# Performance work log

Measured on AMD Instinct MI355X. Metric: run time of the kernel, lower is better.

Reference implementation:

```python
import jax, jax.numpy as jnp
import numpy as np

B, HIST, T_TOTAL = 16, 8, 16
C, IN_DIM, EMB, HID = 1000, 16, 32, 64
E = 16000
D_BASE = 2
ED = D_BASE + 3                # edge_dim = 5
IN_CONV = IN_DIM - 1 + EMB + 2  # 49
IN_GRU = IN_CONV + HID          # 113
N = B * C
U10_MEAN, U10_STD = 0.5, 3.0
V10_MEAN, V10_STD = -0.3, 3.0
TWO_PI = 2.0 * np.pi


def _wind_dir(u, v):
    # metpy wind_direction in radians: 90deg - atan2(-v,-u), wrapped to (0, 2pi], calm -> 0
    d = jnp.pi / 2 - jnp.arctan2(-v, -u)
    d = jnp.where(d <= 0, d + TWO_PI, d)
    return jnp.where(jnp.hypot(u, v) == 0, 0.0, d)


def setup_inputs():
    key = jax.random.key(0)
    ks = jax.random.split(key, 32)
    X = jax.random.normal(ks[0], (B, T_TOTAL, C, IN_DIM), jnp.float32)
    node_ids = jnp.broadcast_to(jnp.arange(C, dtype=jnp.float32), (B, T_TOTAL, C))
    X = X.at[..., -1].set(node_ids)  # last column = node id (embedding index)
    y = jax.random.normal(ks[1], (B, T_TOTAL, C, 1), jnp.float32)
    edge_indices = jax.random.randint(ks[2], (2, E), 0, C, jnp.int32)
    dist = jax.random.uniform(ks[3], (E,), jnp.float32, 10.0, 100.0)
    direc = jax.random.uniform(ks[4], (E,), jnp.float32, 0.0, TWO_PI)
    edge_attr0 = jnp.stack([dist, direc], axis=-1)

    def lin(k, fin, fout):
        s = 1.0 / np.sqrt(fin)
        return jax.random.uniform(k, (fin, fout), jnp.float32, -s, s)

    def bias(k, fout):
        return jax.random.normal(k, (fout,), jnp.float32) * 0.01

    return {
        'X': X, 'y': y, 'edge_attr0': edge_attr0,
        'emb_table': jax.random.normal(ks[5], (C, EMB), jnp.float32),
        'Wq': lin(ks[6], IN_CONV, HID), 'bq': bias(ks[7], HID),
        'Wk': lin(ks[8], IN_CONV, HID), 'bk': bias(ks[9], HID),
        'Wv': lin(ks[10], IN_CONV, HID), 'bv': bias(ks[11], HID),
        'We': lin(ks[12], ED, HID), 'be': bias(ks[13], HID),
        'Wskip': lin(ks[14], IN_CONV, HID), 'bskip': bias(ks[15], HID),
        'W_ih': lin(ks[16], IN_GRU, 3 * HID).T, 'b_ih': bias(ks[17], 3 * HID),
        'W_hh': lin(ks[18], HID, 3 * HID).T, 'b_hh': bias(ks[19], 3 * HID),
        'Wout': lin(ks[20], HID, 1), 'bout': bias(ks[21], 1),
        'edge_indices': edge_indices,
    }


def reference(X, y, edge_attr0, emb_table, Wq, bq, Wk, bk, Wv, bv, We, be,
              Wskip, bskip, W_ih, b_ih, W_hh, b_hh, Wout, bout, edge_indices):
    offs = jnp.arange(B, dtype=jnp.int32) * C
    # batched-graph indices, flattened batch-major (b*E+e) exactly as the source
    SRC = (edge_indices[0][None, :] + offs[:, None]).reshape(-1)
    DST = (edge_indices[1][None, :] + offs[:, None]).reshape(-1)
    src_nodes = edge_indices[0]
    base = edge_attr0[src_nodes]  # [E, 2] (dist, dir); faithful to edge_attr[src] quirk
    inv_sqrt_d = 1.0 / np.sqrt(HID)

    def step(carry, xs):
        hn, xn = carry
        Xt, yt = xs  # [B,C,IN_DIM], [B,C,1]
        ids = Xt[..., -1].astype(jnp.int32)
        emb = emb_table[ids]                               # [B,C,EMB]
        feats = Xt[..., :-1]
        x = jnp.concatenate([xn, yt, feats, emb], axis=-1)  # [B,C,IN_CONV]
        # vectorized wind physics (replaces the per-edge CPU loop)
        u10 = feats[..., -2] * U10_STD + U10_MEAN
        v10 = feats[..., -1] * V10_STD + V10_MEAN
        speed = jnp.hypot(u10, v10)
        wind = jnp.stack([speed, _wind_dir(u10, v10)], axis=-1)      # [B,C,2]
        w_e = jnp.transpose(wind[:, src_nodes, :], (1, 0, 2))        # [E,B,2]
        base_e = jnp.broadcast_to(base[:, None, :], (E, B, D_BASE))
        attr4 = jnp.concatenate([base_e, w_e], axis=-1)              # [E,B,4]
        theta = jnp.abs(attr4[..., 1] - attr4[..., 3])
        adv = jax.nn.relu(3.0 * attr4[..., 2] * jnp.cos(theta) / attr4[..., 0])
        # edge-major flatten (e*B+b), paired with batch-major SRC/DST as in source
        edge_attr = jnp.concatenate([attr4, adv[..., None]], axis=-1).reshape(E * B, ED)
        # TransformerConv, heads=1, eval (no dropout)
        xf = x.reshape(N, IN_CONV)
        q = xf @ Wq + bq
        kk = xf @ Wk + bk
        vv = xf @ Wv + bv
        e_emb = edge_attr @ We + be
        k_e = kk[SRC] + e_emb
        v_e = vv[SRC] + e_emb
        alpha = jnp.sum(q[DST] * k_e, axis=-1) * inv_sqrt_d
        m = jax.ops.segment_max(alpha, DST, num_segments=N)
        a = jnp.exp(alpha - m[DST])
        s = jax.ops.segment_sum(a, DST, num_segments=N)
        p = a / s[DST]
        out = jax.ops.segment_sum(p[:, None] * v_e, DST, num_segments=N)
        out = out + xf @ Wskip + bskip
        x_gcn = jax.nn.sigmoid(out).reshape(B, C, HID)
        x2 = jnp.concatenate([x, x_gcn], axis=-1).reshape(N, IN_GRU)
        # GRUCell
        gi = x2 @ W_ih.T + b_ih
        gh = hn @ W_hh.T + b_hh
        i_r, i_z, i_n = jnp.split(gi, 3, axis=-1)
        h_r, h_z, h_n = jnp.split(gh, 3, axis=-1)
        r = jax.nn.sigmoid(i_r + h_r)
        z = jax.nn.sigmoid(i_z + h_z)
        n = jnp.tanh(i_n + r * h_n)
        hn_new = (1.0 - z) * n + z * hn
        xn_new = hn_new.reshape(B, C, HID) @ Wout + bout
        return (hn_new, xn_new), None

    hn0 = jnp.zeros((N, HID), jnp.float32)
    xn0 = jnp.zeros((B, C, 1), jnp.float32)
    xs = (jnp.swapaxes(X[:, :HIST], 0, 1), jnp.swapaxes(y[:, :HIST], 0, 1))
    (hn, xn), _ = jax.lax.scan(step, (hn0, xn0), xs)
    return hn, xn
```

## Files before the change

### kernel.cpp

```cpp
#include <hip/hip_runtime.h>
#include <math.h>

#define B_ 16
#define T_TOT 16
#define C_ 1000
#define N_ 16000
#define E_ 16000
#define HID 64
#define EMB 32
#define IN_DIM 16
#define XF 17
#define HIST 8
#define SXP 160
#define HOFF 96
#define SHP 168
#define SGP 268
#define Q_ 16

typedef __attribute__((ext_vector_type(8))) short bf16x8;
typedef __attribute__((ext_vector_type(4))) float f32x4;

__device__ __forceinline__ float sigmoidf_(float x) { return 1.f / (1.f + expf(-x)); }

__global__ void k_init(float* __restrict__ hn, float* __restrict__ xn, int* __restrict__ cnt) {
  int total = N_ * HID + N_ + C_;
  for (int i = blockIdx.x * 256 + threadIdx.x; i < total; i += gridDim.x * 256) {
    if (i < N_ * HID) hn[i] = 0.f;
    else if (i < N_ * HID + N_) xn[i - N_ * HID] = 0.f;
    else cnt[i - N_ * HID - N_] = 0;
  }
}

__global__ void k_prep(const float* __restrict__ W_ih, const float* __restrict__ W_hh,
                       unsigned short* __restrict__ WBhi, unsigned short* __restrict__ WBlo,
                       float* __restrict__ WihT2) {
  int i = blockIdx.x * 256 + threadIdx.x;
  if (i < 30720) {
    const int j = i & 7;
    const int l = (i >> 3) & 63;
    const int ksnt = i >> 9;
    const int ks = ksnt % 5, nt = ksnt / 5;
    const int k = ks * 32 + (l >> 4) * 8 + j;
    const int g = nt * 16 + (l & 15);
    float w = 0.f;
    if (k < 17) w = W_ih[g * 113 + k];
    else if (k < 81) w = W_ih[g * 113 + 49 + (k - 17)];
    else if (k >= HOFF) w = W_hh[g * 64 + (k - HOFF)];
    const unsigned ub = __float_as_uint(w);
    const float hif = __uint_as_float(ub & 0xffff0000u);
    WBhi[i] = (unsigned short)(ub >> 16);
    WBlo[i] = (unsigned short)(__float_as_uint(w - hif) >> 16);
  } else if (i < 30720 + 32 * 192) {
    int i2 = i - 30720;
    int j2 = i2 / 192, g = i2 - j2 * 192;
    WihT2[i2] = W_ih[g * 113 + 17 + j2];
  }
}

__global__ __launch_bounds__(256) void k_embfold(
    const float* __restrict__ emb_table,
    const float* __restrict__ Wq, const float* __restrict__ Wk,
    const float* __restrict__ Wv, const float* __restrict__ Wskip,
    const float* __restrict__ WihT2,
    float* __restrict__ embW, float* __restrict__ gihemb) {
  __shared__ float se[EMB];
  const int c = blockIdx.x;
  const int t = threadIdx.x;
  if (t < EMB) se[t] = emb_table[c * EMB + t];
  __syncthreads();
  const int mat = t >> 6, h = t & 63;
  const float* Wm = (mat == 0) ? Wq : (mat == 1) ? Wk : (mat == 2) ? Wv : Wskip;
  float acc = 0.f;
#pragma unroll
  for (int j = 0; j < EMB; ++j) acc = fmaf(se[j], Wm[(17 + j) * HID + h], acc);
  embW[c * 256 + t] = acc;
  if (t < 192) {
    float a2 = 0.f;
#pragma unroll
    for (int j = 0; j < EMB; ++j) a2 = fmaf(se[j], WihT2[j * 192 + t], a2);
    gihemb[c * 192 + t] = a2;
  }
}

__global__ __launch_bounds__(256) void k_count(const int* __restrict__ dst,
                                               int* __restrict__ qcnt, int* __restrict__ cnt) {
  const int gw = (blockIdx.x * 256 + threadIdx.x) >> 6;
  const int lane = threadIdx.x & 63;
  const int d = gw >> 4, q = gw & (Q_ - 1);
  const int e0 = q * (E_ / Q_);
  int cur = 0;
  for (int base = 0; base < E_ / Q_; base += 64) {
    const bool in = (base + lane) < (E_ / Q_);
    const int e = e0 + (in ? base + lane : 0);
    cur += __popcll(__ballot(in && (dst[e] == d)));
  }
  if (lane == 0) { qcnt[(d << 4) + q] = cur; atomicAdd(&cnt[d], cur); }
}

__global__ __launch_bounds__(1024) void k_scan(const int* __restrict__ cnt, int* __restrict__ rowptr) {
  __shared__ int s[1024];
  int t = threadIdx.x;
  s[t] = (t < C_) ? cnt[t] : 0;
  __syncthreads();
  for (int off = 1; off < 1024; off <<= 1) {
    int v = (t >= off) ? s[t - off] : 0;
    __syncthreads();
    s[t] += v;
    __syncthreads();
  }
  if (t < C_) rowptr[t + 1] = s[t];
  if (t == 0) rowptr[0] = 0;
}

__global__ __launch_bounds__(256) void k_scatter(const int* __restrict__ dst,
                                                 const int* __restrict__ rowptr,
                                                 const int* __restrict__ qcnt,
                                                 int* __restrict__ csr_e) {
  const int gw = (blockIdx.x * 256 + threadIdx.x) >> 6;
  const int lane = threadIdx.x & 63;
  const int d = gw >> 4, q = gw & (Q_ - 1);
  int cur = rowptr[d];
  for (int qq = 0; qq < q; ++qq) cur += qcnt[(d << 4) + qq];
  const int e0 = q * (E_ / Q_);
  for (int base = 0; base < E_ / Q_; base += 64) {
    const bool in = (base + lane) < (E_ / Q_);
    const int e = e0 + (in ? base + lane : 0);
    const bool pred = in && (dst[e] == d);
    const unsigned long long mask = __ballot(pred);
    if (pred) csr_e[cur + __popcll(mask & ((1ull << lane) - 1))] = e;
    cur += __popcll(mask);
  }
}

__global__ __launch_bounds__(256) void k_pack(const int* __restrict__ src,
                                              const int* __restrict__ csr_e,
                                              const float* __restrict__ ea0,
                                              int4* __restrict__ pack) {
  const int idx = blockIdx.x * 256 + threadIdx.x;
  const int b = idx / E_, j = idx - b * E_;
  const int e = csr_e[j];
  const int se = src[b * 1000 + (e >> 4)];
  int4 rec;
  rec.x = b * C_ + src[e];
  rec.y = (e & 15) * C_ + se;
  rec.z = __float_as_int(ea0[2 * se]);
  rec.w = __float_as_int(ea0[2 * se + 1]);
  pack[idx] = rec;
}

__global__ __launch_bounds__(256) void k_node_pre(
    const float* __restrict__ X, const float* __restrict__ y,
    const float* __restrict__ embW,
    const float* __restrict__ Wk, const float* __restrict__ bk,
    const float* __restrict__ Wv, const float* __restrict__ bv,
    const float* __restrict__ xn_prev,
    float* __restrict__ k, float* __restrict__ v, float2* __restrict__ wind, int t)
{
  __shared__ float sx[4][XF];
  const int local = threadIdx.x >> 6;
  const int h = threadIdx.x & 63;
  const int n = blockIdx.x * 4 + local;
  const int b = n / C_, c = n % C_;
  const float* Xrow = X + (((b * T_TOT + t) * C_ + c) * IN_DIM);

  if (h == 0)       sx[local][0] = xn_prev[n];
  else if (h == 1)  sx[local][1] = y[(b * T_TOT + t) * C_ + c];
  else if (h <= 16) sx[local][h] = Xrow[h - 2];
  if (h == 0) {
    float u10 = Xrow[13] * 3.0f + 0.5f;
    float v10 = Xrow[14] * 3.0f - 0.3f;
    float sp = hypotf(u10, v10);
    float dd = 1.5707963267948966f - atan2f(-v10, -u10);
    if (dd <= 0.f) dd += 6.283185307179586f;
    if (sp == 0.f) dd = 0.f;
    wind[n] = make_float2(sp, dd);
  }
  __syncthreads();

  const float* eW = embW + c * 256;
  float ak = bk[h] + eW[64 + h];
  float av = bv[h] + eW[128 + h];
#pragma unroll
  for (int j = 0; j < XF; ++j) {
    const float xv = sx[local][j];
    ak = fmaf(xv, Wk[j * HID + h], ak);
    av = fmaf(xv, Wv[j * HID + h], av);
  }
  k[(size_t)n * HID + h] = ak;
  v[(size_t)n * HID + h] = av;
}

__global__ __launch_bounds__(256, 4) void k_node_main(
    const int* __restrict__ rowptr, const int4* __restrict__ pack,
    const float* __restrict__ X, const float* __restrict__ y,
    const float* __restrict__ xn_prev,
    const float* __restrict__ embW, const float* __restrict__ gihemb,
    const float* __restrict__ Wq, const float* __restrict__ bq,
    const float* __restrict__ Wskip, const float* __restrict__ bskip,
    const float* __restrict__ Wk, const float* __restrict__ bk,
    const float* __restrict__ Wv, const float* __restrict__ bv,
    const float* __restrict__ We, const float* __restrict__ be,
    const float* __restrict__ kR, const float* __restrict__ vR, const float2* __restrict__ windR,
    float* __restrict__ kW, float* __restrict__ vW, float2* __restrict__ windW,
    const unsigned short* __restrict__ WBhi, const unsigned short* __restrict__ WBlo,
    const float* __restrict__ b_ih, const float* __restrict__ b_hh,
    const float* __restrict__ Wout, const float* __restrict__ bout,
    const float* __restrict__ hn_in, float* __restrict__ hn_out, float* __restrict__ xn_out,
    int t, int last)
{
  __shared__ float sxh[16 * SXP];
  __shared__ unsigned short sxhH[16 * SHP];
  __shared__ unsigned short sxhL[16 * SHP];
  __shared__ float sg[16 * SGP];

  const int h = threadIdx.x & 63;
  const int wv = threadIdx.x >> 6;
  const int grp = h >> 4, t16 = h & 15;
  const int gbase = h & 48;
  const int lb = ((int)blockIdx.x & 7) * 125 + ((int)blockIdx.x >> 3);
  const int nb0 = wv * 4;
  const int nloc = nb0 + grp;
  const int n = lb * 16 + nloc;
  const int b = n / C_, d = n % C_;

  const int r0 = rowptr[d];
  const int deg = rowptr[d + 1] - r0;
  const int4* packb = pack + (size_t)b * E_;

#pragma unroll 1
  for (int i = 0; i < 4; ++i) {
    const int nl = nb0 + i;
    const int ng = lb * 16 + nl;
    const int bb = ng / C_, cc = ng % C_;
    const float* Xrow = X + (((size_t)(bb * T_TOT + t) * C_ + cc) * IN_DIM);
    float* row = &sxh[nl * SXP];
    if (h == 0)       row[0] = xn_prev[ng];
    else if (h == 1)  row[1] = y[(size_t)(bb * T_TOT + t) * C_ + cc];
    else if (h <= 16) row[h] = Xrow[h - 2];
  }

  float4 qv4, sk4, pA, pB;
  {
    const float* eW = embW + d * 256;
    {
      const float4 bq4 = *(const float4*)(bq + t16 * 4);
      const float4 eq4 = *(const float4*)(eW + t16 * 4);
      qv4 = make_float4(bq4.x + eq4.x, bq4.y + eq4.y, bq4.z + eq4.z, bq4.w + eq4.w);
      const float4 bs4 = *(const float4*)(bskip + t16 * 4);
      const float4 es4 = *(const float4*)(eW + 192 + t16 * 4);
      sk4 = make_float4(bs4.x + es4.x, bs4.y + es4.y, bs4.z + es4.z, bs4.w + es4.w);
    }
    const float* row = &sxh[nloc * SXP];
#pragma unroll 4
    for (int j = 0; j < XF; ++j) {
      const float xv = row[j];
      const float4 wq = *(const float4*)(Wq + j * HID + t16 * 4);
      const float4 ws = *(const float4*)(Wskip + j * HID + t16 * 4);
      qv4.x = fmaf(xv, wq.x, qv4.x); qv4.y = fmaf(xv, wq.y, qv4.y);
      qv4.z = fmaf(xv, wq.z, qv4.z); qv4.w = fmaf(xv, wq.w, qv4.w);
      sk4.x = fmaf(xv, ws.x, sk4.x); sk4.y = fmaf(xv, ws.y, sk4.y);
      sk4.z = fmaf(xv, ws.z, sk4.z); sk4.w = fmaf(xv, ws.w, sk4.w);
    }
    const float4 bee = *(const float4*)(be + t16 * 4);
    const float4 w0 = *(const float4*)(We + t16 * 4);
    const float4 w1 = *(const float4*)(We + 64 + t16 * 4);
    const float4 w2 = *(const float4*)(We + 128 + t16 * 4);
    const float4 w3 = *(const float4*)(We + 192 + t16 * 4);
    const float4 w4 = *(const float4*)(We + 256 + t16 * 4);
    float p0 = qv4.x * bee.x + qv4.y * bee.y + qv4.z * bee.z + qv4.w * bee.w;
    float p1 = qv4.x * w0.x + qv4.y * w0.y + qv4.z * w0.z + qv4.w * w0.w;
    float p2 = qv4.x * w1.x + qv4.y * w1.y + qv4.z * w1.z + qv4.w * w1.w;
    float p3 = qv4.x * w2.x + qv4.y * w2.y + qv4.z * w2.z + qv4.w * w2.w;
    float p4 = qv4.x * w3.x + qv4.y * w3.y + qv4.z * w3.z + qv4.w * w3.w;
    float p5 = qv4.x * w4.x + qv4.y * w4.y + qv4.z * w4.z + qv4.w * w4.w;
#pragma unroll
    for (int off = 1; off < 16; off <<= 1) {
      p0 += __shfl_xor(p0, off); p1 += __shfl_xor(p1, off); p2 += __shfl_xor(p2, off);
      p3 += __shfl_xor(p3, off); p4 += __shfl_xor(p4, off); p5 += __shfl_xor(p5, off);
    }
    pA = make_float4(p0, p1, p2, p3);
    pB = make_float4(p4, p5, 0.f, 0.f);
  }

  float m = -INFINITY, s = 0.f, S1 = 0.f, S2 = 0.f, S3 = 0.f, S4 = 0.f, S5 = 0.f;
  float4 o4 = make_float4(0.f, 0.f, 0.f, 0.f);

  for (int cb = 0; cb < deg; cb += 16) {
    const int nb = min(16, deg - cb);
    const int4 rec = packb[r0 + cb + (t16 < nb ? t16 : 0)];
    const int nsrc = rec.x;
    const float dist = __int_as_float(rec.z), dirc = __int_as_float(rec.w);
    const float2 w2w = windR[rec.y];
    const float sp = w2w.x, wd = w2w.y;
    const float adv = fmaxf(0.f, 3.f * sp * cosf(fabsf(dirc - wd)) / dist);
    float asc = pA.x;
    asc = fmaf(dist, pA.y, asc); asc = fmaf(dirc, pA.z, asc); asc = fmaf(sp, pA.w, asc);
    asc = fmaf(wd, pB.x, asc);   asc = fmaf(adv, pB.y, asc);

    float alpha = -INFINITY;
#pragma unroll 4
    for (int j = 0; j < nb; ++j) {
      const int sl = gbase | j;
      const int nsb = __shfl(nsrc, sl);
      const float4 kv = *(const float4*)(kR + (size_t)nsb * HID + t16 * 4);
      float part = qv4.x * kv.x + qv4.y * kv.y + qv4.z * kv.z + qv4.w * kv.w;
      part += __shfl_xor(part, 1);
      part += __shfl_xor(part, 2);
      part += __shfl_xor(part, 4);
      part += __shfl_xor(part, 8);
      const float af = (part + __shfl(asc, sl)) * 0.125f;
      if (t16 == j) alpha = af;
    }

    float mx = alpha;
    mx = fmaxf(mx, __shfl_xor(mx, 1));
    mx = fmaxf(mx, __shfl_xor(mx, 2));
    mx = fmaxf(mx, __shfl_xor(mx, 4));
    mx = fmaxf(mx, __shfl_xor(mx, 8));
    const float mnew = fmaxf(m, mx);
    const float scale = expf(m - mnew);
    const float a = expf(alpha - mnew);
    float ra = a, q1 = a * dist, q2 = a * dirc, q3 = a * sp, q4 = a * wd, q5 = a * adv;
#pragma unroll
    for (int off = 1; off < 16; off <<= 1) {
      ra += __shfl_xor(ra, off); q1 += __shfl_xor(q1, off); q2 += __shfl_xor(q2, off);
      q3 += __shfl_xor(q3, off); q4 += __shfl_xor(q4, off); q5 += __shfl_xor(q5, off);
    }
    s  = s * scale + ra;  S1 = S1 * scale + q1; S2 = S2 * scale + q2;
    S3 = S3 * scale + q3; S4 = S4 * scale + q4; S5 = S5 * scale + q5;
    o4.x *= scale; o4.y *= scale; o4.z *= scale; o4.w *= scale;
    m = mnew;

#pragma unroll 4
    for (int j = 0; j < nb; ++j) {
      const int sl = gbase | j;
      const float aj = __shfl(a, sl);
      const int nsb = __shfl(nsrc, sl);
      const float4 v4 = *(const float4*)(vR + (size_t)nsb * HID + t16 * 4);
      o4.x = fmaf(aj, v4.x, o4.x); o4.y = fmaf(aj, v4.y, o4.y);
      o4.z = fmaf(aj, v4.z, o4.z); o4.w = fmaf(aj, v4.w, o4.w);
    }
  }

  {
    const float4 be4 = *(const float4*)(be + t16 * 4);
    const float4 e0 = *(const float4*)(We + t16 * 4);
    const float4 e1 = *(const float4*)(We + 64 + t16 * 4);
    const float4 e2 = *(const float4*)(We + 128 + t16 * 4);
    const float4 e3 = *(const float4*)(We + 192 + t16 * 4);
    const float4 e4 = *(const float4*)(We + 256 + t16 * 4);
    const float inv = (s > 0.f) ? 1.f / s : 0.f;
    float* xr = &sxh[nloc * SXP];
    float ox, oy, oz, ow;
    ox = s * be4.x; ox = fmaf(S1, e0.x, ox); ox = fmaf(S2, e1.x, ox); ox = fmaf(S3, e2.x, ox); ox = fmaf(S4, e3.x, ox); ox = fmaf(S5, e4.x, ox);
    oy = s * be4.y; oy = fmaf(S1, e0.y, oy); oy = fmaf(S2, e1.y, oy); oy = fmaf(S3, e2.y, oy); oy = fmaf(S4, e3.y, oy); oy = fmaf(S5, e4.y, oy);
    oz = s * be4.z; oz = fmaf(S1, e0.z, oz); oz = fmaf(S2, e1.z, oz); oz = fmaf(S3, e2.z, oz); oz = fmaf(S4, e3.z, oz); oz = fmaf(S5, e4.z, oz);
    ow = s * be4.w; ow = fmaf(S1, e0.w, ow); ow = fmaf(S2, e1.w, ow); ow = fmaf(S3, e2.w, ow); ow = fmaf(S4, e3.w, ow); ow = fmaf(S5, e4.w, ow);
    xr[17 + t16 * 4 + 0] = sigmoidf_(sk4.x + (o4.x + ox) * inv);
    xr[17 + t16 * 4 + 1] = sigmoidf_(sk4.y + (o4.y + oy) * inv);
    xr[17 + t16 * 4 + 2] = sigmoidf_(sk4.z + (o4.z + oz) * inv);
    xr[17 + t16 * 4 + 3] = sigmoidf_(sk4.w + (o4.w + ow) * inv);
    const float4 hv4 = *(const float4*)(hn_in + (size_t)n * HID + t16 * 4);
    *(float4*)(&xr[HOFF + t16 * 4]) = hv4;
    if (t16 < 15) xr[81 + t16] = 0.f;
  }

  __syncthreads();
  for (int idx = threadIdx.x; idx < 16 * SXP; idx += 256) {
    const int nd = idx / SXP, rw = idx - nd * SXP;
    const float xv = sxh[idx];
    const unsigned ub = __float_as_uint(xv);
    const float hif = __uint_as_float(ub & 0xffff0000u);
    sxhH[nd * SHP + rw] = (unsigned short)(ub >> 16);
    sxhL[nd * SHP + rw] = (unsigned short)(__float_as_uint(xv - hif) >> 16);
  }
  __syncthreads();

  {
    const int lane = h;
    const int aoff = t16 * SHP + grp * 8;
#pragma unroll 1
    for (int q = 0; q < 3; ++q) {
      const int nt = wv * 3 + q;
      const unsigned short* bhp = WBhi + ((size_t)(nt * 5) * 64 + lane) * 8;
      const unsigned short* blp = WBlo + ((size_t)(nt * 5) * 64 + lane) * 8;
      const int gc = nt * 16 + t16;
      const int nbase = grp * 4;
      if (nt < 8) {
        f32x4 acc = {0.f, 0.f, 0.f, 0.f};
#pragma unroll 1
        for (int ks = 0; ks < 5; ++ks) {
          const bf16x8 Ah = *(const bf16x8*)(&sxhH[aoff + ks * 32]);
          const bf16x8 Al = *(const bf16x8*)(&sxhL[aoff + ks * 32]);
          const bf16x8 Bh = *(const bf16x8*)(bhp + (size_t)ks * 512);
          const bf16x8 Bl = *(const bf16x8*)(blp + (size_t)ks * 512);
          acc = __builtin_amdgcn_mfma_f32_16x16x32_bf16(Ah, Bh, acc, 0, 0, 0);
          acc = __builtin_amdgcn_mfma_f32_16x16x32_bf16(Ah, Bl, acc, 0, 0, 0);
          acc = __builtin_amdgcn_mfma_f32_16x16x32_bf16(Al, Bh, acc, 0, 0, 0);
        }
#pragma unroll
        for (int r = 0; r < 4; ++r) sg[(nbase + r) * SGP + gc] = acc[r];
      } else {
        f32x4 accX = {0.f, 0.f, 0.f, 0.f};
        f32x4 accH = {0.f, 0.f, 0.f, 0.f};
#pragma unroll 1
        for (int ks = 0; ks < 3; ++ks) {
          const bf16x8 Ah = *(const bf16x8*)(&sxhH[aoff + ks * 32]);
          const bf16x8 Al = *(const bf16x8*)(&sxhL[aoff + ks * 32]);
          const bf16x8 Bh = *(const bf16x8*)(bhp + (size_t)ks * 512);
          const bf16x8 Bl = *(const bf16x8*)(blp + (size_t)ks * 512);
          accX = __builtin_amdgcn_mfma_f32_16x16x32_bf16(Ah, Bh, accX, 0, 0, 0);
          accX = __builtin_amdgcn_mfma_f32_16x16x32_bf16(Ah, Bl, accX, 0, 0, 0);
          accX = __builtin_amdgcn_mfma_f32_16x16x32_bf16(Al, Bh, accX, 0, 0, 0);
        }
#pragma unroll 1
        for (int ks = 3; ks < 5; ++ks) {
          const bf16x8 Ah = *(const bf16x8*)(&sxhH[aoff + ks * 32]);
          const bf16x8 Al = *(const bf16x8*)(&sxhL[aoff + ks * 32]);
          const bf16x8 Bh = *(const bf16x8*)(bhp + (size_t)ks * 512);
          const bf16x8 Bl = *(const bf16x8*)(blp + (size_t)ks * 512);
          accH = __builtin_amdgcn_mfma_f32_16x16x32_bf16(Ah, Bh, accH, 0, 0, 0);
          accH = __builtin_amdgcn_mfma_f32_16x16x32_bf16(Ah, Bl, accH, 0, 0, 0);
          accH = __builtin_amdgcn_mfma_f32_16x16x32_bf16(Al, Bh, accH, 0, 0, 0);
        }
        const int gx = 128 + (nt - 8) * 16 + t16;
#pragma unroll
        for (int r = 0; r < 4; ++r) {
          sg[(nbase + r) * SGP + gx] = accX[r];
          sg[(nbase + r) * SGP + gx + 64] = accH[r];
        }
      }
    }
  }
  __syncthreads();

  const float wo = Wout[h];
  const float bout0 = bout[0];
  const float bi0 = b_ih[h] + b_hh[h];
  const float bi1 = b_ih[64 + h] + b_hh[64 + h];
  const float bx = b_ih[128 + h], bh2 = b_hh[128 + h];
#pragma unroll 1
  for (int i = 0; i < 4; ++i) {
    const int nl = nb0 + i;
    const int ng = lb * 16 + nl;
    const int ci = ng % C_;
    const float* ge = gihemb + (size_t)ci * 192;
    const float rg = sigmoidf_(sg[nl * SGP + h] + bi0 + ge[h]);
    const float zg = sigmoidf_(sg[nl * SGP + 64 + h] + bi1 + ge[64 + h]);
    const float gxv = sg[nl * SGP + 128 + h] + bx + ge[128 + h];
    const float ghv = sg[nl * SGP + 192 + h] + bh2;
    const float hv = sxh[nl * SXP + HOFF + h];
    const float nn2 = tanhf(fmaf(rg, ghv, gxv));
    const float hnew = (1.f - zg) * nn2 + zg * hv;
    hn_out[(size_t)ng * HID + h] = hnew;
    float prod = hnew * wo;
#pragma unroll
    for (int off = 1; off < 64; off <<= 1) prod += __shfl_xor(prod, off);
    if (h == 0) {
      const float xnv = prod + bout0;
      xn_out[ng] = xnv;
      sxh[nl * SXP + 0] = xnv;
    }
  }

  if (!last) {
    const int t1 = t + 1;
#pragma unroll 1
    for (int i = 0; i < 4; ++i) {
      const int nl = nb0 + i;
      const int ng = lb * 16 + nl;
      const int bb = ng / C_, cc = ng % C_;
      const float* Xrow = X + (((size_t)(bb * T_TOT + t1) * C_ + cc) * IN_DIM);
      float* row = &sxh[nl * SXP];
      if (h == 1)                 row[1] = y[(size_t)(bb * T_TOT + t1) * C_ + cc];
      else if (h >= 2 && h <= 16) row[h] = Xrow[h - 2];
      if (h == 0) {
        float u10 = Xrow[13] * 3.0f + 0.5f;
        float v10 = Xrow[14] * 3.0f - 0.3f;
        float sp = hypotf(u10, v10);
        float dd = 1.5707963267948966f - atan2f(-v10, -u10);
        if (dd <= 0.f) dd += 6.283185307179586f;
        if (sp == 0.f) dd = 0.f;
        windW[ng] = make_float2(sp, dd);
      }
    }
    {
      const float* eW = embW + d * 256;
      float4 kk4, vv4;
      {
        const float4 bk4 = *(const float4*)(bk + t16 * 4);
        const float4 ek4 = *(const float4*)(eW + 64 + t16 * 4);
        kk4 = make_float4(bk4.x + ek4.x, bk4.y + ek4.y, bk4.z + ek4.z, bk4.w + ek4.w);
        const float4 bv4 = *(const float4*)(bv + t16 * 4);
        const float4 ev4 = *(const float4*)(eW + 128 + t16 * 4);
        vv4 = make_float4(bv4.x + ev4.x, bv4.y + ev4.y, bv4.z + ev4.z, bv4.w + ev4.w);
      }
      const float* row = &sxh[nloc * SXP];
#pragma unroll 1
      for (int j = 0; j < XF; ++j) {
        const float xv = row[j];
        const float4 wk = *(const float4*)(Wk + j * HID + t16 * 4);
        const float4 wvv = *(const float4*)(Wv + j * HID + t16 * 4);
        kk4.x = fmaf(xv, wk.x, kk4.x); kk4.y = fmaf(xv, wk.y, kk4.y);
        kk4.z = fmaf(xv, wk.z, kk4.z); kk4.w = fmaf(xv, wk.w, kk4.w);
        vv4.x = fmaf(xv, wvv.x, vv4.x); vv4.y = fmaf(xv, wvv.y, vv4.y);
        vv4.z = fmaf(xv, wvv.z, vv4.z); vv4.w = fmaf(xv, wvv.w, vv4.w);
      }
      *(float4*)(kW + (size_t)n * HID + t16 * 4) = kk4;
      *(float4*)(vW + (size_t)n * HID + t16 * 4) = vv4;
    }
  }
}

extern "C" void kernel_launch(void* const* d_in, const int* in_sizes, int n_in,
                              void* d_out, int out_size, void* d_ws, size_t ws_size,
                              hipStream_t stream) {
  const float* X      = (const float*)d_in[0];
  const float* y      = (const float*)d_in[1];
  const float* ea0    = (const float*)d_in[2];
  const float* emb    = (const float*)d_in[3];
  const float* Wq     = (const float*)d_in[4];
  const float* bq     = (const float*)d_in[5];
  const float* Wk     = (const float*)d_in[6];
  const float* bk     = (const float*)d_in[7];
  const float* Wv     = (const float*)d_in[8];
  const float* bv     = (const float*)d_in[9];
  const float* We     = (const float*)d_in[10];
  const float* be     = (const float*)d_in[11];
  const float* Wskip  = (const float*)d_in[12];
  const float* bskip  = (const float*)d_in[13];
  const float* W_ih   = (const float*)d_in[14];
  const float* b_ih   = (const float*)d_in[15];
  const float* W_hh   = (const float*)d_in[16];
  const float* b_hh   = (const float*)d_in[17];
  const float* Wout   = (const float*)d_in[18];
  const float* bout   = (const float*)d_in[19];
  const int*   eidx   = (const int*)d_in[20];
  const int* src = eidx;
  const int* dst = eidx + E_;

  float* W = (float*)d_ws;
  size_t off = 0;
  float* kA    = W + off; off += (size_t)N_ * HID;
  float* kB    = W + off; off += (size_t)N_ * HID;
  float* vA    = W + off; off += (size_t)N_ * HID;
  float* vB    = W + off; off += (size_t)N_ * HID;
  float2* wiA  = (float2*)(W + off); off += (size_t)N_ * 2;
  float2* wiB  = (float2*)(W + off); off += (size_t)N_ * 2;
  float* hnA   = W + off; off += (size_t)N_ * HID;
  float* xnA   = W + off; off += N_;
  unsigned short* WBhi = (unsigned short*)(W + off); off += 30720 / 2;
  unsigned short* WBlo = (unsigned short*)(W + off); off += 30720 / 2;
  float* WihT2 = W + off; off += 32 * 192;
  float* embW  = W + off; off += (size_t)C_ * 256;
  float* gihemb= W + off; off += (size_t)C_ * 192;
  off = (off + 3) & ~(size_t)3;
  int4* pack   = (int4*)(W + off); off += (size_t)B_ * E_ * 4;
  int* cnt     = (int*)(W + off); off += C_;
  int* rowptr  = (int*)(W + off); off += C_ + 1;
  int* qcnt    = (int*)(W + off); off += C_ * Q_;
  int* csr_e   = (int*)(W + off); off += E_;

  k_init<<<1024, 256, 0, stream>>>(hnA, xnA, cnt);
  k_prep<<<(30720 + 32 * 192 + 255) / 256, 256, 0, stream>>>(W_ih, W_hh, WBhi, WBlo, WihT2);
  k_embfold<<<C_, 256, 0, stream>>>(emb, Wq, Wk, Wv, Wskip, WihT2, embW, gihemb);
  k_count<<<C_ * Q_ / 4, 256, 0, stream>>>(dst, qcnt, cnt);
  k_scan<<<1, 1024, 0, stream>>>(cnt, rowptr);
  k_scatter<<<C_ * Q_ / 4, 256, 0, stream>>>(dst, rowptr, qcnt, csr_e);
  k_pack<<<B_ * E_ / 256, 256, 0, stream>>>(src, csr_e, ea0, pack);

  float* hn_final = (float*)d_out;
  float* xn_final = (float*)d_out + (size_t)N_ * HID;

  k_node_pre<<<N_ / 4, 256, 0, stream>>>(X, y, embW, Wk, bk, Wv, bv,
                                         xnA, kA, vA, wiA, 0);

  for (int t = 0; t < HIST; ++t) {
    const bool last = (t == HIST - 1);
    const bool even = ((t & 1) == 0);
    k_node_main<<<N_ / 16, 256, 0, stream>>>(rowptr, pack, X, y, xnA, embW, gihemb,
                                             Wq, bq, Wskip, bskip, Wk, bk, Wv, bv, We, be,
                                             even ? kA : kB, even ? vA : vB, even ? wiA : wiB,
                                             even ? kB : kA, even ? vB : vA, even ? wiB : wiA,
                                             WBhi, WBlo,
                                             b_ih, b_hh, Wout, bout,
                                             hnA,
                                             last ? hn_final : hnA,
                                             last ? xn_final : xnA,
                                             t, last ? 1 : 0);
  }
}
```

Baseline: 389.6 us.

## Split edge aggregation across two wave halves with online-softmax merge

The block is doubled to 512 threads. Two groups of four waves each process alternating 16-edge chunks of every node's neighbour list, and their running softmax state (max, sum, weighted sums, output) is merged through shared memory. The GRU MFMA tiles, gate work and next-step k/v projections are redistributed across the eight waves, with k and v split between the halves. This aims to shorten the latency-bound gather loop for each node, at the cost of extra barriers, shared-memory merge traffic and duplicated q/skip projection work in both halves.

Measured after the change: 523.0 us. 1.34x slower.

```diff
diff --git a/kernel.cpp b/kernel.cpp
--- a/kernel.cpp
+++ b/kernel.cpp
@@ -190,7 +190,7 @@
   v[(size_t)n * HID + h] = av;
 }
 
-__global__ __launch_bounds__(256, 4) void k_node_main(
+__global__ __launch_bounds__(512, 6) void k_node_main(
     const int* __restrict__ rowptr, const int4* __restrict__ pack,
     const float* __restrict__ X, const float* __restrict__ y,
     const float* __restrict__ xn_prev,
@@ -215,10 +215,12 @@
 
   const int h = threadIdx.x & 63;
   const int wv = threadIdx.x >> 6;
+  const int par = wv >> 2;
+  const int wq = wv & 3;
   const int grp = h >> 4, t16 = h & 15;
   const int gbase = h & 48;
   const int lb = ((int)blockIdx.x & 7) * 125 + ((int)blockIdx.x >> 3);
-  const int nb0 = wv * 4;
+  const int nb0 = wq * 4;
   const int nloc = nb0 + grp;
   const int n = lb * 16 + nloc;
   const int b = n / C_, d = n % C_;
@@ -227,17 +229,20 @@
   const int deg = rowptr[d + 1] - r0;
   const int4* packb = pack + (size_t)b * E_;
 
-#pragma unroll 1
-  for (int i = 0; i < 4; ++i) {
-    const int nl = nb0 + i;
-    const int ng = lb * 16 + nl;
-    const int bb = ng / C_, cc = ng % C_;
-    const float* Xrow = X + (((size_t)(bb * T_TOT + t) * C_ + cc) * IN_DIM);
-    float* row = &sxh[nl * SXP];
-    if (h == 0)       row[0] = xn_prev[ng];
-    else if (h == 1)  row[1] = y[(size_t)(bb * T_TOT + t) * C_ + cc];
-    else if (h <= 16) row[h] = Xrow[h - 2];
-  }
+  if (par == 0) {
+#pragma unroll 1
+    for (int i = 0; i < 4; ++i) {
+      const int nl = nb0 + i;
+      const int ng = lb * 16 + nl;
+      const int bb = ng / C_, cc = ng % C_;
+      const float* Xrow = X + (((size_t)(bb * T_TOT + t) * C_ + cc) * IN_DIM);
+      float* row = &sxh[nl * SXP];
+      if (h == 0)       row[0] = xn_prev[ng];
+      else if (h == 1)  row[1] = y[(size_t)(bb * T_TOT + t) * C_ + cc];
+      else if (h <= 16) row[h] = Xrow[h - 2];
+    }
+  }
+  __syncthreads();
 
   float4 qv4, sk4, pA, pB;
   {
@@ -254,10 +259,10 @@
 #pragma unroll 4
     for (int j = 0; j < XF; ++j) {
       const float xv = row[j];
-      const float4 wq = *(const float4*)(Wq + j * HID + t16 * 4);
+      const float4 wq4 = *(const float4*)(Wq + j * HID + t16 * 4);
       const float4 ws = *(const float4*)(Wskip + j * HID + t16 * 4);
-      qv4.x = fmaf(xv, wq.x, qv4.x); qv4.y = fmaf(xv, wq.y, qv4.y);
-      qv4.z = fmaf(xv, wq.z, qv4.z); qv4.w = fmaf(xv, wq.w, qv4.w);
+      qv4.x = fmaf(xv, wq4.x, qv4.x); qv4.y = fmaf(xv, wq4.y, qv4.y);
+      qv4.z = fmaf(xv, wq4.z, qv4.z); qv4.w = fmaf(xv, wq4.w, qv4.w);
       sk4.x = fmaf(xv, ws.x, sk4.x); sk4.y = fmaf(xv, ws.y, sk4.y);
       sk4.z = fmaf(xv, ws.z, sk4.z); sk4.w = fmaf(xv, ws.w, sk4.w);
     }
@@ -285,7 +290,7 @@
   float m = -INFINITY, s = 0.f, S1 = 0.f, S2 = 0.f, S3 = 0.f, S4 = 0.f, S5 = 0.f;
   float4 o4 = make_float4(0.f, 0.f, 0.f, 0.f);
 
-  for (int cb = 0; cb < deg; cb += 16) {
+  for (int cb = par * 16; cb < deg; cb += 32) {
     const int nb = min(16, deg - cb);
     const int4 rec = packb[r0 + cb + (t16 < nb ? t16 : 0)];
     const int nsrc = rec.x;
@@ -342,7 +347,31 @@
     }
   }
 
-  {
+  if (par == 1) {
+    float* mg = &sg[nloc * SGP];
+    mg[t16 * 4 + 0] = o4.x; mg[t16 * 4 + 1] = o4.y;
+    mg[t16 * 4 + 2] = o4.z; mg[t16 * 4 + 3] = o4.w;
+    if (t16 == 0) {
+      mg[64] = m; mg[65] = s; mg[66] = S1; mg[67] = S2;
+      mg[68] = S3; mg[69] = S4; mg[70] = S5;
+    }
+  }
+  __syncthreads();
+
+  if (par == 0) {
+    const float* mg = &sg[nloc * SGP];
+    const float mB = mg[64], sB = mg[65];
+    const float mM = fmaxf(m, mB);
+    const float eA = (s  > 0.f) ? expf(m  - mM) : 0.f;
+    const float eB = (sB > 0.f) ? expf(mB - mM) : 0.f;
+    const float4 oB = *(const float4*)(mg + t16 * 4);
+    s  = s * eA + sB * eB;
+    S1 = S1 * eA + mg[66] * eB; S2 = S2 * eA + mg[67] * eB;
+    S3 = S3 * eA + mg[68] * eB; S4 = S4 * eA + mg[69] * eB;
+    S5 = S5 * eA + mg[70] * eB;
+    o4.x = o4.x * eA + oB.x * eB; o4.y = o4.y * eA + oB.y * eB;
+    o4.z = o4.z * eA + oB.z * eB; o4.w = o4.w * eA + oB.w * eB;
+
     const float4 be4 = *(const float4*)(be + t16 * 4);
     const float4 e0 = *(const float4*)(We + t16 * 4);
     const float4 e1 = *(const float4*)(We + 64 + t16 * 4);
@@ -364,9 +393,9 @@
     *(float4*)(&xr[HOFF + t16 * 4]) = hv4;
     if (t16 < 15) xr[81 + t16] = 0.f;
   }
-
-  __syncthreads();
-  for (int idx = threadIdx.x; idx < 16 * SXP; idx += 256) {
+  __syncthreads();
+
+  for (int idx = threadIdx.x; idx < 16 * SXP; idx += 512) {
     const int nd = idx / SXP, rw = idx - nd * SXP;
     const float xv = sxh[idx];
     const unsigned ub = __float_as_uint(xv);
@@ -380,11 +409,9 @@
     const int lane = h;
     const int aoff = t16 * SHP + grp * 8;
 #pragma unroll 1
-    for (int q = 0; q < 3; ++q) {
-      const int nt = wv * 3 + q;
+    for (int nt = wv; nt < 12; nt += 8) {
       const unsigned short* bhp = WBhi + ((size_t)(nt * 5) * 64 + lane) * 8;
       const unsigned short* blp = WBlo + ((size_t)(nt * 5) * 64 + lane) * 8;
-      const int gc = nt * 16 + t16;
       const int nbase = grp * 4;
       if (nt < 8) {
         f32x4 acc = {0.f, 0.f, 0.f, 0.f};
@@ -398,6 +425,7 @@
           acc = __builtin_amdgcn_mfma_f32_16x16x32_bf16(Ah, Bl, acc, 0, 0, 0);
           acc = __builtin_amdgcn_mfma_f32_16x16x32_bf16(Al, Bh, acc, 0, 0, 0);
         }
+        const int gc = nt * 16 + t16;
 #pragma unroll
         for (int r = 0; r < 4; ++r) sg[(nbase + r) * SGP + gc] = acc[r];
       } else {
@@ -440,8 +468,8 @@
   const float bi1 = b_ih[64 + h] + b_hh[64 + h];
   const float bx = b_ih[128 + h], bh2 = b_hh[128 + h];
 #pragma unroll 1
-  for (int i = 0; i < 4; ++i) {
-    const int nl = nb0 + i;
+  for (int i = 0; i < 2; ++i) {
+    const int nl = wv * 2 + i;
     const int ng = lb * 16 + nl;
     const int ci = ng % C_;
     const float* ge = gihemb + (size_t)ci * 192;
@@ -465,49 +493,58 @@
 
   if (!last) {
     const int t1 = t + 1;
-#pragma unroll 1
-    for (int i = 0; i < 4; ++i) {
-      const int nl = nb0 + i;
-      const int ng = lb * 16 + nl;
-      const int bb = ng / C_, cc = ng % C_;
-      const float* Xrow = X + (((size_t)(bb * T_TOT + t1) * C_ + cc) * IN_DIM);
-      float* row = &sxh[nl * SXP];
-      if (h == 1)                 row[1] = y[(size_t)(bb * T_TOT + t1) * C_ + cc];
-      else if (h >= 2 && h <= 16) row[h] = Xrow[h - 2];
-      if (h == 0) {
-        float u10 = Xrow[13] * 3.0f + 0.5f;
-        float v10 = Xrow[14] * 3.0f - 0.3f;
-        float sp = hypotf(u10, v10);
-        float dd = 1.5707963267948966f - atan2f(-v10, -u10);
-        if (dd <= 0.f) dd += 6.283185307179586f;
-        if (sp == 0.f) dd = 0.f;
-        windW[ng] = make_float2(sp, dd);
+    if (par == 0) {
+#pragma unroll 1
+      for (int i = 0; i < 4; ++i) {
+        const int nl = nb0 + i;
+        const int ng = lb * 16 + nl;
+        const int bb = ng / C_, cc = ng % C_;
+        const float* Xrow = X + (((size_t)(bb * T_TOT + t1) * C_ + cc) * IN_DIM);
+        float* row = &sxh[nl * SXP];
+        if (h == 1)                 row[1] = y[(size_t)(bb * T_TOT + t1) * C_ + cc];
+        else if (h >= 2 && h <= 16) row[h] = Xrow[h - 2];
+        if (h == 0) {
+          float u10 = Xrow[13] * 3.0f + 0.5f;
+          float v10 = Xrow[14] * 3.0f - 0.3f;
+          float sp = hypotf(u10, v10);
+          float dd = 1.5707963267948966f - atan2f(-v10, -u10);
+          if (dd <= 0.f) dd += 6.283185307179586f;
+          if (sp == 0.f) dd = 0.f;
+          windW[ng] = make_float2(sp, dd);
+        }
       }
     }
+    __syncthreads();
     {
       const float* eW = embW + d * 256;
-      float4 kk4, vv4;
-      {
+      const float* row = &sxh[nloc * SXP];
+      if (par == 0) {
+        float4 kk4;
         const float4 bk4 = *(const float4*)(bk + t16 * 4);
         const float4 ek4 = *(const float4*)(eW + 64 + t16 * 4);
         kk4 = make_float4(bk4.x + ek4.x, bk4.y + ek4.y, bk4.z + ek4.z, bk4.w + ek4.w);
+#pragma unroll 1
+        for (int j = 0; j < XF; ++j) {
+          const float xv = row[j];
+          const float4 wk = *(const float4*)(Wk + j * HID + t16 * 4);
+          kk4.x = fmaf(xv, wk.x, kk4.x); kk4.y = fmaf(xv, wk.y, kk4.y);
+          kk4.z = fmaf(xv, wk.z, kk4.z); kk4.w = fmaf(xv, wk.w, kk4.w);
+        }
+        *(float4*)(kW + (size_t)n * HID + t16 * 4) = kk4;
+      } else {
+        float4 vv4;
         const float4 bv4 = *(const float4*)(bv + t16 * 4);
         const float4 ev4 = *(const float4*)(eW + 128 + t16 * 4);
         vv4 = make_float4(bv4.x + ev4.x, bv4.y + ev4.y, bv4.z + ev4.z, bv4.w + ev4.w);
+#pragma unroll 1
+        for (int j = 0; j < XF; ++j) {
+          const float xv = row[j];
+          const float4 wvv = *(const float4*)(Wv + j * HID + t16 * 4);
+          vv4.x = fmaf(xv, wvv.x, vv4.x); vv4.y = fmaf(xv, wvv.y, vv4.y);
+          vv4.z = fmaf(xv, wvv.z, vv4.z); vv4.w = fmaf(xv, wvv.w, vv4.w);
+        }
+        *(float4*)(vW + (size_t)n * HID + t16 * 4) = vv4;
       }
-      const float* row = &sxh[nloc * SXP];
-#pragma unroll 1
-      for (int j = 0; j < XF; ++j) {
-        const float xv = row[j];
-        const float4 wk = *(const float4*)(Wk + j * HID + t16 * 4);
-        const float4 wvv = *(const float4*)(Wv + j * HID + t16 * 4);
-        kk4.x = fmaf(xv, wk.x, kk4.x); kk4.y = fmaf(xv, wk.y, kk4.y);
-        kk4.z = fmaf(xv, wk.z, kk4.z); kk4.w = fmaf(xv, wk.w, kk4.w);
-        vv4.x = fmaf(xv, wvv.x, vv4.x); vv4.y = fmaf(xv, wvv.y, vv4.y);
-        vv4.z = fmaf(xv, wvv.z, vv4.z); vv4.w = fmaf(xv, wvv.w, vv4.w);
-      }
-      *(float4*)(kW + (size_t)n * HID + t16 * 4) = kk4;
-      *(float4*)(vW + (size_t)n * HID + t16 * 4) = vv4;
     }
   }
 }
@@ -578,7 +615,7 @@
   for (int t = 0; t < HIST; ++t) {
     const bool last = (t == HIST - 1);
     const bool even = ((t & 1) == 0);
-    k_node_main<<<N_ / 16, 256, 0, stream>>>(rowptr, pack, X, y, xnA, embW, gihemb,
+    k_node_main<<<N_ / 16, 512, 0, stream>>>(rowptr, pack, X, y, xnA, embW, gihemb,
                                              Wq, bq, Wskip, bskip, Wk, bk, Wv, bv, We, be,
                                              even ? kA : kB, even ? vA : vB, even ? wiA : wiB,
                                              even ? kB : kA, even ? vB : vA, even ? wiB : wiA,
```
